# Performance work log

Hardware: AMD Instinct MI355X
Metric: run time of the kernel (lower is better)

The kernel has to match this reference:

```python
import jax, jax.numpy as jnp
import numpy as np

N_NODES = 100000
N_EDGES = 1600000
NFEAT = 128
NHID = 128
NCLS = 40


def _glorot(key, shape):
    fan_in, fan_out = shape[1], shape[0]
    lim = (6.0 / (fan_in + fan_out)) ** 0.5
    return jax.random.uniform(key, shape, jnp.float32, -lim, lim)


def setup_inputs() -> dict:
    key = jax.random.key(0)
    ks = jax.random.split(key, 10)
    x = jax.random.normal(ks[0], (N_NODES, NFEAT), jnp.float32)
    edge_index = jax.random.randint(ks[1], (2, N_EDGES), 0, N_NODES, jnp.int64)
    return {
        "x": x,
        "edge_index": edge_index,
        # SAGEConv layer 0: lin_l (neighbor aggr, with bias) and lin_r (root)
        "W_l0": _glorot(ks[2], (NHID, NFEAT)),
        "b_l0": jnp.zeros((NHID,), jnp.float32),
        "W_r0": _glorot(ks[3], (NHID, NFEAT)),
        # SAGEConv layer 1
        "W_l1": _glorot(ks[4], (NHID, NHID)),
        "b_l1": jnp.zeros((NHID,), jnp.float32),
        "W_r1": _glorot(ks[5], (NHID, NHID)),
        # classifier
        "W_cls": _glorot(ks[6], (NCLS, NHID)),
        "b_cls": jnp.zeros((NCLS,), jnp.float32),
    }


def _sage_conv(x, src, dst, deg_inv, W_l, b_l, W_r):
    # gather source-node features along edges, mean-aggregate at targets
    msgs = x[src]                                            # [E, d_in]
    aggr = jax.ops.segment_sum(msgs, dst, num_segments=N_NODES)  # [N, d_in]
    aggr = aggr * deg_inv[:, None]                           # mean
    # out = lin_l(aggr) + lin_r(x)
    return aggr @ W_l.T + b_l + x @ W_r.T


def reference(x, edge_index, W_l0, b_l0, W_r0, W_l1, b_l1, W_r1, W_cls, b_cls):
    src, dst = edge_index[0], edge_index[1]
    deg = jax.ops.segment_sum(jnp.ones((src.shape[0],), x.dtype), dst,
                              num_segments=N_NODES)
    deg_inv = 1.0 / jnp.maximum(deg, 1.0)

    h = jax.nn.relu(_sage_conv(x, src, dst, deg_inv, W_l0, b_l0, W_r0))
    h = jax.nn.relu(_sage_conv(h, src, dst, deg_inv, W_l1, b_l1, W_r1))
    return h @ W_cls.T + b_cls  # [N, ncls]
```

## Files before the change

### kernel.cpp

```cpp
#include <hip/hip_runtime.h>

#define NN 100000
#define NE 1600000
#define DD 128
#define NCLS_ 40
#define PAD 64
#define NPART 8
#define PSZ 12500
#define PBLK 250
#define ECHUNK 6400
#define NITER 25

typedef unsigned short u16;
typedef unsigned int u32;
typedef __attribute__((ext_vector_type(2))) unsigned int u32x2;
typedef __attribute__((ext_vector_type(8))) short short8;
typedef __attribute__((ext_vector_type(4))) float f32x4;

static __device__ __forceinline__ u16 f2b(float f) {
  u32 u = __float_as_uint(f);
  u32 r = (u + 0x7FFFu + ((u >> 16) & 1u)) >> 16;
  return (u16)r;
}

__global__ void k_flag(const int* __restrict__ ei, int* __restrict__ flag) {
  __shared__ int nz;
  if (threadIdx.x == 0) nz = 0;
  __syncthreads();
  if (threadIdx.x < 512) {
    int w = ei[2 * threadIdx.x + 1];
    if (w != 0) atomicOr(&nz, 1);
  }
  __syncthreads();
  if (threadIdx.x == 0) flag[0] = (nz == 0) ? 1 : 0;
}

static __device__ __forceinline__ int eget_nt(const int* ei, int pos, int is64) {
  return is64 ? __builtin_nontemporal_load(ei + 2 * (size_t)pos)
              : __builtin_nontemporal_load(ei + pos);
}

static __device__ __forceinline__ void cvt1(const float* __restrict__ s,
                                            u16* __restrict__ d, int j) {
  float4 v;
  v.x = __builtin_nontemporal_load((const float*)s + 4 * (size_t)j + 0);
  v.y = __builtin_nontemporal_load((const float*)s + 4 * (size_t)j + 1);
  v.z = __builtin_nontemporal_load((const float*)s + 4 * (size_t)j + 2);
  v.w = __builtin_nontemporal_load((const float*)s + 4 * (size_t)j + 3);
  u32x2 pk;
  pk.x = (u32)f2b(v.x) | ((u32)f2b(v.y) << 16);
  pk.y = (u32)f2b(v.z) | ((u32)f2b(v.w) << 16);
  __builtin_nontemporal_store(pk, (u32x2*)d + j);
}

__global__ __launch_bounds__(256) void k_prep(
    const int* __restrict__ ei, const int* __restrict__ flag,
    int* __restrict__ cnt, int* __restrict__ csrp,
    const float* __restrict__ x, u16* __restrict__ xb,
    const float* __restrict__ w0, const float* __restrict__ w1,
    const float* __restrict__ w2, const float* __restrict__ w3,
    u16* __restrict__ o0, u16* __restrict__ o1,
    u16* __restrict__ o2, u16* __restrict__ o3,
    const float* __restrict__ wc, u16* __restrict__ wcb) {
  int is64 = flag[0];
  int g = blockIdx.x & (NPART - 1);
  int sub = blockIdx.x >> 3;
  int e0 = sub * ECHUNK;
  int lo = g * PSZ;
  int gtid = blockIdx.x * 256 + threadIdx.x;
#pragma unroll 1
  for (int it = 0; it < NITER; ++it) {
    int e = e0 + it * 256 + threadIdx.x;
    int dst = eget_nt(ei, NE + e, is64);
    if ((u32)(dst - lo) < (u32)PSZ) {
      int src = eget_nt(ei, e, is64);
      int r = atomicAdd(&cnt[dst], 1);
      if (r < PAD) csrp[dst * PAD + r] = src;
    }
    if (it < 7) {
      int i = it * 512000 + gtid;
      if (i < NN * DD / 4) cvt1(x, xb, i);
    } else if (it == 7) {
      if (gtid < 4 * 4096) {
        int which = gtid >> 12, j = gtid & 4095;
        const float* s = which == 0 ? w0 : which == 1 ? w1 : which == 2 ? w2 : w3;
        u16* d = which == 0 ? o0 : which == 1 ? o1 : which == 2 ? o2 : o3;
        cvt1(s, d, j);
      } else if (gtid < 4 * 4096 + 6144) {
        int i = gtid - 4 * 4096;
        float v = (i < NCLS_ * DD) ? wc[i] : 0.f;
        wcb[i] = f2b(v);
      }
    }
  }
}

__global__ __launch_bounds__(256, 2) void k_aggr(
    const u16* __restrict__ in, const int* __restrict__ csrp,
    const int* __restrict__ cnt, u16* __restrict__ out) {
  int wid = blockIdx.x * 4 + (threadIdx.x >> 6);
  if (wid >= NN) return;
  int lane = threadIdx.x & 63;
  int l16 = lane & 15;
  int deg = cnt[wid];
  int nb = deg > PAD ? PAD : deg;
  const u32* in32 = (const u32*)in;
  const int* seg = csrp + (size_t)wid * PAD;
  float a0 = 0.f, a1 = 0.f;
  int full = nb >> 4;
  for (int b = 0; b < full; b++) {
    int c = seg[b * 16 + l16];
    u32 v[16];
#pragma unroll
    for (int k = 0; k < 16; k++) {
      int sk = __builtin_amdgcn_readlane(c, k);
      v[k] = in32[(size_t)sk * 64 + lane];
    }
#pragma unroll
    for (int k = 0; k < 16; k++) {
      a0 += __uint_as_float(v[k] << 16);
      a1 += __uint_as_float(v[k] & 0xFFFF0000u);
    }
  }
  int done = full << 4;
  int rem = nb - done;
  if (rem) {
    int c = seg[done + (l16 < rem ? l16 : 0)];
    u32 v[16];
#pragma unroll
    for (int k = 0; k < 16; k++) {
      if (k < rem) {
        int sk = __builtin_amdgcn_readlane(c, k);
        v[k] = in32[(size_t)sk * 64 + lane];
      }
    }
#pragma unroll
    for (int k = 0; k < 16; k++) {
      if (k < rem) {
        a0 += __uint_as_float(v[k] << 16);
        a1 += __uint_as_float(v[k] & 0xFFFF0000u);
      }
    }
  }
  float sc = 1.0f / (float)(deg > 1 ? deg : 1);
  a0 *= sc;
  a1 *= sc;
  u32 pk = (u32)f2b(a0) | ((u32)f2b(a1) << 16);
  ((u32*)out)[(size_t)wid * 64 + lane] = pk;
}

template <int NT, bool RELU, bool F32OUT, bool HASR>
__global__ __launch_bounds__(256) void k_layer(
    const u16* A1, const u16* A2,
    const u16* __restrict__ WL, const u16* __restrict__ WR,
    const float* __restrict__ bias, void* out, int ncols) {
  int wv = blockIdx.x * 4 + (threadIdx.x >> 6);
  int base = wv * 16;
  if (base >= NN) return;
  int lane = threadIdx.x & 63;
  int m = lane & 15, kg = lane >> 4;
  f32x4 acc[NT];
#pragma unroll
  for (int t = 0; t < NT; t++) acc[t] = (f32x4){0.f, 0.f, 0.f, 0.f};
#pragma unroll
  for (int kk = 0; kk < 4; kk++) {
    int ko = kk * 32 + kg * 8;
    short8 aA = *(const short8*)(A1 + (size_t)(base + m) * DD + ko);
    short8 aX;
    if constexpr (HASR) aX = *(const short8*)(A2 + (size_t)(base + m) * DD + ko);
#pragma unroll
    for (int t = 0; t < NT; t++) {
      short8 bL = *(const short8*)(WL + (size_t)(t * 16 + m) * DD + ko);
      acc[t] = __builtin_amdgcn_mfma_f32_16x16x32_bf16(aA, bL, acc[t], 0, 0, 0);
      if constexpr (HASR) {
        short8 bR = *(const short8*)(WR + (size_t)(t * 16 + m) * DD + ko);
        acc[t] = __builtin_amdgcn_mfma_f32_16x16x32_bf16(aX, bR, acc[t], 0, 0, 0);
      }
    }
  }
#pragma unroll
  for (int t = 0; t < NT; t++) {
    int o = t * 16 + m;
#pragma unroll
    for (int r = 0; r < 4; r++) {
      int node = base + kg * 4 + r;
      float v = acc[t][r];
      if (o < ncols) v += bias[o];
      if constexpr (RELU) v = fmaxf(v, 0.f);
      if constexpr (F32OUT) {
        if (o < ncols) ((float*)out)[(size_t)node * ncols + o] = v;
      } else {
        ((u16*)out)[(size_t)node * DD + o] = f2b(v);
      }
    }
  }
}

extern "C" void kernel_launch(void* const* d_in, const int* in_sizes, int n_in,
                              void* d_out, int out_size, void* d_ws, size_t ws_size,
                              hipStream_t stream) {
  const float* x = (const float*)d_in[0];
  const int* ei = (const int*)d_in[1];
  const float* wl0 = (const float*)d_in[2];
  const float* bl0 = (const float*)d_in[3];
  const float* wr0 = (const float*)d_in[4];
  const float* wl1 = (const float*)d_in[5];
  const float* bl1 = (const float*)d_in[6];
  const float* wr1 = (const float*)d_in[7];
  const float* wcls = (const float*)d_in[8];
  const float* bcls = (const float*)d_in[9];

  char* ws = (char*)d_ws;
  size_t off = 0;
  auto alloc = [&](size_t b) {
    size_t r = off;
    off += (b + 255) & ~(size_t)255;
    return r;
  };
  int* flag = (int*)(ws + alloc(4));
  int* cnt = (int*)(ws + alloc((size_t)NN * 4));
  int* csrp = (int*)(ws + alloc((size_t)NN * PAD * 4));
  u16* xb = (u16*)(ws + alloc((size_t)NN * DD * 2));
  u16* h0 = (u16*)(ws + alloc((size_t)NN * DD * 2));
  u16* ag = (u16*)(ws + alloc((size_t)NN * DD * 2));
  u16* wl0b = (u16*)(ws + alloc((size_t)DD * DD * 2));
  u16* wr0b = (u16*)(ws + alloc((size_t)DD * DD * 2));
  u16* wl1b = (u16*)(ws + alloc((size_t)DD * DD * 2));
  u16* wr1b = (u16*)(ws + alloc((size_t)DD * DD * 2));
  u16* wclsb = (u16*)(ws + alloc((size_t)48 * DD * 2));
  if (off > ws_size) return;

  (void)hipMemsetAsync(cnt, 0, (size_t)NN * 4, stream);
  k_flag<<<1, 512, 0, stream>>>(ei, flag);
  k_prep<<<NPART * PBLK, 256, 0, stream>>>(ei, flag, cnt, csrp,
                                           x, xb, wl0, wr0, wl1, wr1,
                                           wl0b, wr0b, wl1b, wr1b, wcls, wclsb);

  const int LB = (NN + 63) / 64;

  k_aggr<<<NN / 4, 256, 0, stream>>>(xb, csrp, cnt, ag);
  k_layer<8, true, false, true><<<LB, 256, 0, stream>>>(ag, xb, wl0b, wr0b, bl0, h0, DD);
  k_aggr<<<NN / 4, 256, 0, stream>>>(h0, csrp, cnt, ag);
  k_layer<8, true, false, true><<<LB, 256, 0, stream>>>(ag, h0, wl1b, wr1b, bl1, ag, DD);
  k_layer<3, false, true, false><<<LB, 256, 0, stream>>>(ag, nullptr, wclsb, nullptr, bcls, d_out, NCLS_);
}
```

Before: 350.6 us.

## Fuse neighbor aggregation with SAGE linear layers and classifier via LDS tiles

Merges the mean-aggregation kernel with the following dual-matrix MFMA layer. Each block aggregates 16 nodes into a swizzled LDS tile and then runs the GEMM straight from LDS, so the bf16 aggregate buffer is no longer written to and read back from global memory. The second layer also folds the classifier GEMM into the same kernel through a second LDS tile, cutting five launches to two. In exchange, each wave now aggregates 4 nodes serially before a block barrier, which lowers gather parallelism per block and may add load imbalance from varying node degrees. Only one wave runs the classifier MFMA.

```diff
diff --git a/kernel.cpp b/kernel.cpp
--- a/kernel.cpp
+++ b/kernel.cpp
@@ -95,102 +95,132 @@
   }
 }
 
-__global__ __launch_bounds__(256, 2) void k_aggr(
+template <bool LAST>
+__global__ __launch_bounds__(256, 2) void k_fused(
     const u16* __restrict__ in, const int* __restrict__ csrp,
-    const int* __restrict__ cnt, u16* __restrict__ out) {
-  int wid = blockIdx.x * 4 + (threadIdx.x >> 6);
-  if (wid >= NN) return;
+    const int* __restrict__ cnt,
+    const u16* __restrict__ WL, const u16* __restrict__ WR,
+    const float* __restrict__ bias,
+    u16* __restrict__ hout,
+    const u16* __restrict__ Wc, const float* __restrict__ bc,
+    float* __restrict__ out) {
+  __shared__ u32 agt[16 * 64];
+  __shared__ u32 h1t[LAST ? 16 * 64 : 1];
+  int wv = threadIdx.x >> 6;
   int lane = threadIdx.x & 63;
   int l16 = lane & 15;
-  int deg = cnt[wid];
-  int nb = deg > PAD ? PAD : deg;
+  int base16 = blockIdx.x * 16;
   const u32* in32 = (const u32*)in;
-  const int* seg = csrp + (size_t)wid * PAD;
-  float a0 = 0.f, a1 = 0.f;
-  int full = nb >> 4;
-  for (int b = 0; b < full; b++) {
-    int c = seg[b * 16 + l16];
-    u32 v[16];
-#pragma unroll
-    for (int k = 0; k < 16; k++) {
-      int sk = __builtin_amdgcn_readlane(c, k);
-      v[k] = in32[(size_t)sk * 64 + lane];
-    }
-#pragma unroll
-    for (int k = 0; k < 16; k++) {
-      a0 += __uint_as_float(v[k] << 16);
-      a1 += __uint_as_float(v[k] & 0xFFFF0000u);
-    }
-  }
-  int done = full << 4;
-  int rem = nb - done;
-  if (rem) {
-    int c = seg[done + (l16 < rem ? l16 : 0)];
-    u32 v[16];
-#pragma unroll
-    for (int k = 0; k < 16; k++) {
-      if (k < rem) {
+
+  for (int j = 0; j < 4; j++) {
+    int nl = wv * 4 + j;
+    int wid = base16 + nl;
+    int deg = cnt[wid];
+    int nb = deg > PAD ? PAD : deg;
+    const int* seg = csrp + (size_t)wid * PAD;
+    float a0 = 0.f, a1 = 0.f;
+    int full = nb >> 4;
+    for (int b = 0; b < full; b++) {
+      int c = seg[b * 16 + l16];
+      u32 v[16];
+#pragma unroll
+      for (int k = 0; k < 16; k++) {
         int sk = __builtin_amdgcn_readlane(c, k);
         v[k] = in32[(size_t)sk * 64 + lane];
       }
-    }
-#pragma unroll
-    for (int k = 0; k < 16; k++) {
-      if (k < rem) {
+#pragma unroll
+      for (int k = 0; k < 16; k++) {
         a0 += __uint_as_float(v[k] << 16);
         a1 += __uint_as_float(v[k] & 0xFFFF0000u);
       }
     }
-  }
-  float sc = 1.0f / (float)(deg > 1 ? deg : 1);
-  a0 *= sc;
-  a1 *= sc;
-  u32 pk = (u32)f2b(a0) | ((u32)f2b(a1) << 16);
-  ((u32*)out)[(size_t)wid * 64 + lane] = pk;
-}
-
-template <int NT, bool RELU, bool F32OUT, bool HASR>
-__global__ __launch_bounds__(256) void k_layer(
-    const u16* A1, const u16* A2,
-    const u16* __restrict__ WL, const u16* __restrict__ WR,
-    const float* __restrict__ bias, void* out, int ncols) {
-  int wv = blockIdx.x * 4 + (threadIdx.x >> 6);
-  int base = wv * 16;
-  if (base >= NN) return;
-  int lane = threadIdx.x & 63;
+    int done = full << 4;
+    int rem = nb - done;
+    if (rem) {
+      int c = seg[done + (l16 < rem ? l16 : 0)];
+      u32 v[16];
+#pragma unroll
+      for (int k = 0; k < 16; k++) {
+        if (k < rem) {
+          int sk = __builtin_amdgcn_readlane(c, k);
+          v[k] = in32[(size_t)sk * 64 + lane];
+        }
+      }
+#pragma unroll
+      for (int k = 0; k < 16; k++) {
+        if (k < rem) {
+          a0 += __uint_as_float(v[k] << 16);
+          a1 += __uint_as_float(v[k] & 0xFFFF0000u);
+        }
+      }
+    }
+    float sc = 1.0f / (float)(deg > 1 ? deg : 1);
+    u32 pk = (u32)f2b(a0 * sc) | ((u32)f2b(a1 * sc) << 16);
+    agt[nl * 64 + (lane ^ ((nl & 7) << 2))] = pk;
+  }
+  __syncthreads();
+
   int m = lane & 15, kg = lane >> 4;
-  f32x4 acc[NT];
-#pragma unroll
-  for (int t = 0; t < NT; t++) acc[t] = (f32x4){0.f, 0.f, 0.f, 0.f};
+  f32x4 acc[2];
+#pragma unroll
+  for (int t = 0; t < 2; t++) acc[t] = (f32x4){0.f, 0.f, 0.f, 0.f};
 #pragma unroll
   for (int kk = 0; kk < 4; kk++) {
     int ko = kk * 32 + kg * 8;
-    short8 aA = *(const short8*)(A1 + (size_t)(base + m) * DD + ko);
-    short8 aX;
-    if constexpr (HASR) aX = *(const short8*)(A2 + (size_t)(base + m) * DD + ko);
-#pragma unroll
-    for (int t = 0; t < NT; t++) {
+    int cu = (ko >> 1) ^ ((m & 7) << 2);
+    short8 aA = *(const short8*)((const u16*)agt + m * 128 + cu * 2);
+    short8 aX = *(const short8*)(in + (size_t)(base16 + m) * DD + ko);
+#pragma unroll
+    for (int tt = 0; tt < 2; tt++) {
+      int t = wv * 2 + tt;
       short8 bL = *(const short8*)(WL + (size_t)(t * 16 + m) * DD + ko);
-      acc[t] = __builtin_amdgcn_mfma_f32_16x16x32_bf16(aA, bL, acc[t], 0, 0, 0);
-      if constexpr (HASR) {
-        short8 bR = *(const short8*)(WR + (size_t)(t * 16 + m) * DD + ko);
-        acc[t] = __builtin_amdgcn_mfma_f32_16x16x32_bf16(aX, bR, acc[t], 0, 0, 0);
-      }
-    }
-  }
-#pragma unroll
-  for (int t = 0; t < NT; t++) {
-    int o = t * 16 + m;
+      acc[tt] = __builtin_amdgcn_mfma_f32_16x16x32_bf16(aA, bL, acc[tt], 0, 0, 0);
+      short8 bR = *(const short8*)(WR + (size_t)(t * 16 + m) * DD + ko);
+      acc[tt] = __builtin_amdgcn_mfma_f32_16x16x32_bf16(aX, bR, acc[tt], 0, 0, 0);
+    }
+  }
+#pragma unroll
+  for (int tt = 0; tt < 2; tt++) {
+    int o = (wv * 2 + tt) * 16 + m;
 #pragma unroll
     for (int r = 0; r < 4; r++) {
-      int node = base + kg * 4 + r;
-      float v = acc[t][r];
-      if (o < ncols) v += bias[o];
-      if constexpr (RELU) v = fmaxf(v, 0.f);
-      if constexpr (F32OUT) {
-        if (o < ncols) ((float*)out)[(size_t)node * ncols + o] = v;
+      int nl = kg * 4 + r;
+      float v = fmaxf(acc[tt][r] + bias[o], 0.f);
+      if constexpr (!LAST) {
+        hout[(size_t)(base16 + nl) * DD + o] = f2b(v);
       } else {
-        ((u16*)out)[(size_t)node * DD + o] = f2b(v);
+        ((u16*)h1t)[nl * 128 + (o ^ ((nl & 7) << 3))] = f2b(v);
+      }
+    }
+  }
+
+  if constexpr (LAST) {
+    __syncthreads();
+    if (wv == 0) {
+      f32x4 ac[3];
+#pragma unroll
+      for (int t = 0; t < 3; t++) ac[t] = (f32x4){0.f, 0.f, 0.f, 0.f};
+#pragma unroll
+      for (int kk = 0; kk < 4; kk++) {
+        int ko = kk * 32 + kg * 8;
+        int cu = (ko >> 1) ^ ((m & 7) << 2);
+        short8 aH = *(const short8*)((const u16*)h1t + m * 128 + cu * 2);
+#pragma unroll
+        for (int t = 0; t < 3; t++) {
+          short8 bC = *(const short8*)(Wc + (size_t)(t * 16 + m) * DD + ko);
+          ac[t] = __builtin_amdgcn_mfma_f32_16x16x32_bf16(aH, bC, ac[t], 0, 0, 0);
+        }
+      }
+#pragma unroll
+      for (int t = 0; t < 3; t++) {
+        int o = t * 16 + m;
+        if (o < NCLS_) {
+#pragma unroll
+          for (int r = 0; r < 4; r++) {
+            int node = base16 + kg * 4 + r;
+            out[(size_t)node * NCLS_ + o] = ac[t][r] + bc[o];
+          }
+        }
       }
     }
   }
@@ -222,7 +252,6 @@
   int* csrp = (int*)(ws + alloc((size_t)NN * PAD * 4));
   u16* xb = (u16*)(ws + alloc((size_t)NN * DD * 2));
   u16* h0 = (u16*)(ws + alloc((size_t)NN * DD * 2));
-  u16* ag = (u16*)(ws + alloc((size_t)NN * DD * 2));
   u16* wl0b = (u16*)(ws + alloc((size_t)DD * DD * 2));
   u16* wr0b = (u16*)(ws + alloc((size_t)DD * DD * 2));
   u16* wl1b = (u16*)(ws + alloc((size_t)DD * DD * 2));
@@ -236,11 +265,10 @@
                                            x, xb, wl0, wr0, wl1, wr1,
                                            wl0b, wr0b, wl1b, wr1b, wcls, wclsb);
 
-  const int LB = (NN + 63) / 64;
-
-  k_aggr<<<NN / 4, 256, 0, stream>>>(xb, csrp, cnt, ag);
-  k_layer<8, true, false, true><<<LB, 256, 0, stream>>>(ag, xb, wl0b, wr0b, bl0, h0, DD);
-  k_aggr<<<NN / 4, 256, 0, stream>>>(h0, csrp, cnt, ag);
-  k_layer<8, true, false, true><<<LB, 256, 0, stream>>>(ag, h0, wl1b, wr1b, bl1, ag, DD);
-  k_layer<3, false, true, false><<<LB, 256, 0, stream>>>(ag, nullptr, wclsb, nullptr, bcls, d_out, NCLS_);
-}
+  const int FB = NN / 16;
+
+  k_fused<false><<<FB, 256, 0, stream>>>(xb, csrp, cnt, wl0b, wr0b, bl0,
+                                         h0, nullptr, nullptr, nullptr);
+  k_fused<true><<<FB, 256, 0, stream>>>(h0, csrp, cnt, wl1b, wr1b, bl1,
+                                        nullptr, wclsb, bcls, (float*)d_out);
+}
```

New measurement: 306.2 us. 1.14x faster.
